# Optimization experiments

Hardware: AMD Instinct MI355X
Metric: run time of the kernel (lower is better)

The kernel has to match this reference:

```python
import jax, jax.numpy as jnp
import numpy as np

ALPHA = 1.702
LIMIT = 7.0


def setup_inputs() -> dict:
    key = jax.random.key(0)
    ks = jax.random.split(key, 6)
    A, B, E, M, H = 1, 1, 8, 1024, 2048
    I2 = 4096  # 2 * intermediate_size, interleaved gate/up
    inter = I2 // 2
    return {
        "dispatched": jax.random.normal(ks[0], (A, B, E, M, H), dtype=jnp.float32),
        "w1": jax.random.normal(ks[1], (E, H, I2), dtype=jnp.float32) * 0.02,
        "w1_bias": jax.random.normal(ks[2], (E, I2), dtype=jnp.float32) * 0.02,
        "w2": jax.random.normal(ks[3], (E, inter, H), dtype=jnp.float32) * 0.02,
        "w2_bias": jax.random.normal(ks[4], (E, H), dtype=jnp.float32) * 0.02,
        "sparsity_remap": jax.random.randint(ks[5], (E,), 0, E, dtype=jnp.int32),
        "BD": 1,
        "S": 1024,
    }


def reference(dispatched, w1, w1_bias, w2, w2_bias, sparsity_remap, BD, S):
    # dispatched: [A, B, E, M, H]; w1: [E, H, 2I]; w2: [E, I, H]
    # tt.sparse_matmul == grouped per-expert GEMM; dense math is identical.
    A, Bt, E, M, H = dispatched.shape
    # fused gate+up projection: [A, B, E, M, 2I]
    gu = jnp.einsum("abemh,ehn->abemn", dispatched, w1) + w1_bias[None, None, :, None, :]
    # interleaved gate/up split (gpt_oss activation path)
    gate = gu[..., 0::2]
    up = gu[..., 1::2]
    gate = jnp.minimum(gate, LIMIT)
    up = jnp.clip(up, -LIMIT, LIMIT)
    glu = gate * jax.nn.sigmoid(gate * ALPHA)
    activated = (up + 1.0) * glu  # [A, B, E, M, I]
    inter = activated.shape[-1]
    activated = activated.reshape(A * Bt, E, M, inter)
    # down projection: [A*B, E, M, H]
    down = jnp.einsum("bemi,eih->bemh", activated, w2) + w2_bias[None, :, None, :]
    # permute(1,0,2,3) then untile to [E, 1, BD*S, H]
    out = jnp.transpose(down, (1, 0, 2, 3)).reshape(E, 1, BD * S, H)
    return out
```

## Files before the change

### kernel.cpp

```cpp
#include <hip/hip_runtime.h>
#include <hip/hip_bf16.h>
#include <cstdint>
#include <cstddef>

#define E_ 8
#define M_ 1024
#define H_ 2048
#define I2_ 4096
#define INTER_ 2048

typedef __attribute__((ext_vector_type(8))) __bf16 bf16x8;
typedef __attribute__((ext_vector_type(4))) float f32x4;

__device__ __forceinline__ unsigned short f2bf(float x) {
  union { float f; unsigned u; } v; v.f = x;
  unsigned r = v.u + 0x7fffu + ((v.u >> 16) & 1u);
  return (unsigned short)(r >> 16);
}

__device__ __forceinline__ unsigned pk2(float lo, float hi) {
  __hip_bfloat162 h = __float22bfloat162_rn(make_float2(lo, hi));
  union { __hip_bfloat162 h2; unsigned u; } c; c.h2 = h; return c.u;
}

__device__ __forceinline__ int bofs(int kp, int r) {
  int f = (20 * ((kp >> 2) & 3)) ^ ((kp & 1) << 4);
  return kp * 128 + (r ^ f);
}

__global__ void k_cvt(const float* __restrict__ src, unsigned short* __restrict__ dst, int n4) {
  int i = blockIdx.x * blockDim.x + threadIdx.x;
  int stride = gridDim.x * blockDim.x;
  const float4* s4 = (const float4*)src;
  ushort4* d4 = (ushort4*)dst;
  for (; i < n4; i += stride) {
    float4 v = s4[i];
    ushort4 o;
    o.x = f2bf(v.x); o.y = f2bf(v.y); o.z = f2bf(v.z); o.w = f2bf(v.w);
    d4[i] = o;
  }
}

template<int PERM>
__global__ __launch_bounds__(256) void k_wt(
    const float* __restrict__ W, unsigned short* __restrict__ Wp, int Kd, int Nd) {
  __shared__ float tt[64][65];
  const int tid = threadIdx.x;
  const int e = blockIdx.z;
  const int nb0 = blockIdx.x * 64;
  const int k0 = blockIdx.y * 64;
  const float* We = W + (size_t)e * Kd * Nd;

  #pragma unroll
  for (int i = 0; i < 4; ++i) {
    int r = (tid >> 4) + 16 * i;
    int c4 = tid & 15;
    float4 v = *(const float4*)(We + (size_t)(k0 + r) * Nd + nb0 + 4 * c4);
    tt[r][4 * c4 + 0] = v.x;
    tt[r][4 * c4 + 1] = v.y;
    tt[r][4 * c4 + 2] = v.z;
    tt[r][4 * c4 + 3] = v.w;
  }
  __syncthreads();

  int n = tid >> 2;
  int kc = (tid & 3) * 16;
  int nglob = nb0 + n;
  int nrow;
  if (PERM) {
    int b = nglob >> 5, w = nglob & 31;
    nrow = 32 * b + ((w & 1) ? 16 + (w >> 1) : (w >> 1));
  } else {
    nrow = nglob;
  }
  unsigned o[8];
  #pragma unroll
  for (int j = 0; j < 8; ++j)
    o[j] = pk2(tt[kc + 2 * j][n], tt[kc + 2 * j + 1][n]);
  unsigned short* dst = Wp + (size_t)e * Nd * Kd + (size_t)nrow * Kd + k0 + kc;
  *(uint4*)(dst) = *(uint4*)&o[0];
  *(uint4*)(dst + 8) = *(uint4*)&o[4];
}

template<int ACT, int N, int K>
__global__ __launch_bounds__(256) void k_gemm_nt(
    const unsigned short* __restrict__ A,
    const unsigned short* __restrict__ B,
    const float* __restrict__ bias,
    unsigned short* __restrict__ ActOut,
    float* __restrict__ Out)
{
  __shared__ unsigned short la[128 * 64];
  __shared__ unsigned short lb[128 * 64];
  const int tid = threadIdx.x;
  const int lane = tid & 63;
  const int wv = tid >> 6;
  const int wm = wv & 1, wn = wv >> 1;
  const int e = blockIdx.z;
  const int n0 = blockIdx.x * 128;
  const int m0 = blockIdx.y * 128;
  const unsigned short* Ae = A + (size_t)e * M_ * K + (size_t)m0 * K;
  const unsigned short* Be = B + (size_t)e * N * K + (size_t)n0 * K;

  const unsigned short* ga[4];
  const unsigned short* gb[4];
  int seg[4];
  #pragma unroll
  for (int t = 0; t < 4; ++t) {
    int s = (wv * 4 + t) * 64 + lane;
    int m = s >> 3;
    int j = (s & 7) ^ (m & 7);
    ga[t] = Ae + (size_t)m * K + j * 8;
    gb[t] = Be + (size_t)m * K + j * 8;
    seg[t] = (wv * 4 + t) * 1024;
  }

  const int c = lane & 15;
  const int q = lane >> 4;

  f32x4 acc[4][4];
  const f32x4 zero = {0.f, 0.f, 0.f, 0.f};
  #pragma unroll
  for (int i = 0; i < 4; ++i)
    #pragma unroll
    for (int j = 0; j < 4; ++j) acc[i][j] = zero;

  const int KT = K / 64;
  for (int kt = 0; kt < KT; ++kt) {
    #pragma unroll
    for (int t = 0; t < 4; ++t) {
      __builtin_amdgcn_global_load_lds(
          (const __attribute__((address_space(1))) void*)(const void*)(ga[t] + kt * 64),
          (__attribute__((address_space(3))) void*)(void*)((char*)la + seg[t]), 16, 0, 0);
      __builtin_amdgcn_global_load_lds(
          (const __attribute__((address_space(1))) void*)(const void*)(gb[t] + kt * 64),
          (__attribute__((address_space(3))) void*)(void*)((char*)lb + seg[t]), 16, 0, 0);
    }
    __syncthreads();

    #pragma unroll
    for (int ks = 0; ks < 2; ++ks) {
      bf16x8 av[4], bv[4];
      #pragma unroll
      for (int mi = 0; mi < 4; ++mi) {
        int row = wm * 64 + mi * 16 + c;
        int slot = row * 8 + ((ks * 4 + q) ^ (c & 7));
        av[mi] = *(const bf16x8*)(la + slot * 8);
      }
      #pragma unroll
      for (int ni = 0; ni < 4; ++ni) {
        int row = wn * 64 + ni * 16 + c;
        int slot = row * 8 + ((ks * 4 + q) ^ (c & 7));
        bv[ni] = *(const bf16x8*)(lb + slot * 8);
      }
      #pragma unroll
      for (int mi = 0; mi < 4; ++mi)
        #pragma unroll
        for (int ni = 0; ni < 4; ++ni)
          acc[mi][ni] = __builtin_amdgcn_mfma_f32_16x16x32_bf16(av[mi], bv[ni], acc[mi][ni], 0, 0, 0);
    }
    __syncthreads();
  }

  if (ACT) {
    unsigned short* ActE = ActOut + (size_t)e * M_ * (N / 2);
    const float* be = bias + (size_t)e * N;
    int colbase = n0 + wn * 64;
    #pragma unroll
    for (int p = 0; p < 2; ++p) {
      int rgc = colbase + 32 * p + c;
      int norig = (rgc & ~31) | (c << 1);
      float bg_ = be[norig];
      float bu_ = be[norig + 1];
      int acol = ((rgc >> 5) << 4) + c;
      #pragma unroll
      for (int mi = 0; mi < 4; ++mi) {
        int rowb = m0 + wm * 64 + mi * 16 + q * 4;
        #pragma unroll
        for (int r = 0; r < 4; ++r) {
          float g = acc[mi][2 * p][r] + bg_;
          float u = acc[mi][2 * p + 1][r] + bu_;
          g = fminf(g, 7.0f);
          u = fminf(fmaxf(u, -7.0f), 7.0f);
          float glu = g / (1.0f + __expf(-1.702f * g));
          float a = (u + 1.0f) * glu;
          ActE[(size_t)(rowb + r) * (N / 2) + acol] = f2bf(a);
        }
      }
    }
  } else {
    float* OutE = Out + (size_t)e * M_ * N;
    const float* be = bias + (size_t)e * N;
    #pragma unroll
    for (int ni = 0; ni < 4; ++ni) {
      int col = n0 + wn * 64 + ni * 16 + c;
      float bb = be[col];
      #pragma unroll
      for (int mi = 0; mi < 4; ++mi) {
        int rowb = m0 + wm * 64 + mi * 16 + q * 4;
        #pragma unroll
        for (int r = 0; r < 4; ++r)
          OutE[(size_t)(rowb + r) * N + col] = acc[mi][ni][r] + bb;
      }
    }
  }
}

template<int ACT, int N, int K>
__global__ __launch_bounds__(256) void k_gemm(
    const unsigned short* __restrict__ A,
    const float* __restrict__ Bf,
    const float* __restrict__ bias,
    unsigned short* __restrict__ ActOut,
    float* __restrict__ Out)
{
  __shared__ unsigned short la[128 * 64];
  __shared__ unsigned lb32[32 * 128];
  const int tid = threadIdx.x;
  const int lane = tid & 63;
  const int wv = tid >> 6;
  const int wm = wv & 1, wn = wv >> 1;
  const int e = blockIdx.z;
  const int n0 = blockIdx.x * 128;
  const int m0 = blockIdx.y * 128;
  const unsigned short* Ae = A + (size_t)e * M_ * K + (size_t)m0 * K;
  const float* Be = Bf + (size_t)e * K * N + n0;

  const unsigned short* ga[4];
  int segb[4];
  #pragma unroll
  for (int t = 0; t < 4; ++t) {
    int s = (wv * 4 + t) * 64 + lane;
    int m = s >> 3;
    int j = (s & 7) ^ (m & 7);
    ga[t] = Ae + (size_t)m * K + j * 8;
    segb[t] = (wv * 4 + t) * 1024;
  }

  int kpb, colb, rg;
  if (ACT) {
    kpb = tid >> 4;
    int g = tid & 15;
    colb = 8 * g;
    rg = 32 * (g >> 2) + 4 * (g & 3);
  } else {
    kpb = tid >> 5;
    colb = 4 * (tid & 31);
    rg = colb;
  }
  const float* bg = Be + (size_t)(2 * kpb) * N + colb;

  const int c = lane & 15;
  const int q = lane >> 4;

  f32x4 acc[4][4];
  const f32x4 zero = {0.f, 0.f, 0.f, 0.f};
  #pragma unroll
  for (int i = 0; i < 4; ++i)
    #pragma unroll
    for (int j = 0; j < 4; ++j) acc[i][j] = zero;

  #define LD4(p, off) (*(const float4*)((p) + (off)))

  float4 pb[8];
  {
    const float* p = bg;
    if (ACT) {
      pb[0] = LD4(p, 0);                    pb[1] = LD4(p, 4);
      pb[2] = LD4(p, (size_t)N);            pb[3] = LD4(p, (size_t)N + 4);
      pb[4] = LD4(p, (size_t)32 * N);       pb[5] = LD4(p, (size_t)32 * N + 4);
      pb[6] = LD4(p, (size_t)33 * N);       pb[7] = LD4(p, (size_t)33 * N + 4);
    } else {
      #pragma unroll
      for (int uu = 0; uu < 4; ++uu) {
        pb[2 * uu]     = LD4(p, (size_t)(16 * uu) * N);
        pb[2 * uu + 1] = LD4(p, (size_t)(16 * uu + 1) * N);
      }
    }
  }

  const int KT = K / 64;
  for (int kt = 0; kt < KT; ++kt) {
    #pragma unroll
    for (int t = 0; t < 4; ++t) {
      __builtin_amdgcn_global_load_lds(
          (const __attribute__((address_space(1))) void*)(const void*)(ga[t] + kt * 64),
          (__attribute__((address_space(3))) void*)(void*)((char*)la + segb[t]), 16, 0, 0);
    }
    if (ACT) {
      #pragma unroll
      for (int uu = 0; uu < 2; ++uu) {
        int kp = kpb + 16 * uu;
        float4 a0 = pb[4 * uu], a1 = pb[4 * uu + 1], b0 = pb[4 * uu + 2], b1 = pb[4 * uu + 3];
        uint4 gv, uv;
        gv.x = pk2(a0.x, b0.x); gv.y = pk2(a0.z, b0.z); gv.z = pk2(a1.x, b1.x); gv.w = pk2(a1.z, b1.z);
        uv.x = pk2(a0.y, b0.y); uv.y = pk2(a0.w, b0.w); uv.z = pk2(a1.w, b1.w); uv.w = pk2(a1.w, b1.w);
        uv.z = pk2(a1.y, b1.y);
        *(uint4*)&lb32[bofs(kp, rg)] = gv;
        *(uint4*)&lb32[bofs(kp, rg + 16)] = uv;
      }
    } else {
      #pragma unroll
      for (int uu = 0; uu < 4; ++uu) {
        int kp = kpb + 8 * uu;
        float4 a = pb[2 * uu], b = pb[2 * uu + 1];
        uint4 v;
        v.x = pk2(a.x, b.x); v.y = pk2(a.y, b.y); v.z = pk2(a.z, b.z); v.w = pk2(a.w, b.w);
        *(uint4*)&lb32[bofs(kp, rg)] = v;
      }
    }
    __syncthreads();

    if (kt + 1 < KT) {
      const float* p = bg + (size_t)(kt + 1) * 64 * N;
      if (ACT) {
        pb[0] = LD4(p, 0);                    pb[1] = LD4(p, 4);
        pb[2] = LD4(p, (size_t)N);            pb[3] = LD4(p, (size_t)N + 4);
        pb[4] = LD4(p, (size_t)32 * N);       pb[5] = LD4(p, (size_t)32 * N + 4);
        pb[6] = LD4(p, (size_t)33 * N);       pb[7] = LD4(p, (size_t)33 * N + 4);
      } else {
        #pragma unroll
        for (int uu = 0; uu < 4; ++uu) {
          pb[2 * uu]     = LD4(p, (size_t)(16 * uu) * N);
          pb[2 * uu + 1] = LD4(p, (size_t)(16 * uu + 1) * N);
        }
      }
    }

    #pragma unroll
    for (int ks = 0; ks < 2; ++ks) {
      bf16x8 av[4], bv[4];
      #pragma unroll
      for (int mi = 0; mi < 4; ++mi) {
        int row = wm * 64 + mi * 16 + c;
        int slot = row * 8 + ((ks * 4 + q) ^ (c & 7));
        av[mi] = *(const bf16x8*)(la + slot * 8);
      }
      #pragma unroll
      for (int ni = 0; ni < 4; ++ni) {
        int r = wn * 64 + ni * 16 + c;
        union { unsigned u[4]; bf16x8 v; } t;
        #pragma unroll
        for (int jp = 0; jp < 4; ++jp)
          t.u[jp] = lb32[bofs(ks * 16 + q * 4 + jp, r)];
        bv[ni] = t.v;
      }
      #pragma unroll
      for (int mi = 0; mi < 4; ++mi)
        #pragma unroll
        for (int ni = 0; ni < 4; ++ni)
          acc[mi][ni] = __builtin_amdgcn_mfma_f32_16x16x32_bf16(av[mi], bv[ni], acc[mi][ni], 0, 0, 0);
    }
    __syncthreads();
  }
  #undef LD4

  if (ACT) {
    unsigned short* ActE = ActOut + (size_t)e * M_ * (N / 2);
    const float* be = bias + (size_t)e * N;
    int colbase = n0 + wn * 64;
    #pragma unroll
    for (int p = 0; p < 2; ++p) {
      int rgc = colbase + 32 * p + c;
      int norig = (rgc & ~31) | (c << 1);
      float bg_ = be[norig];
      float bu_ = be[norig + 1];
      int acol = ((rgc >> 5) << 4) + c;
      #pragma unroll
      for (int mi = 0; mi < 4; ++mi) {
        int rowb = m0 + wm * 64 + mi * 16 + q * 4;
        #pragma unroll
        for (int r = 0; r < 4; ++r) {
          float g = acc[mi][2 * p][r] + bg_;
          float u = acc[mi][2 * p + 1][r] + bu_;
          g = fminf(g, 7.0f);
          u = fminf(fmaxf(u, -7.0f), 7.0f);
          float glu = g / (1.0f + __expf(-1.702f * g));
          float a = (u + 1.0f) * glu;
          ActE[(size_t)(rowb + r) * (N / 2) + acol] = f2bf(a);
        }
      }
    }
  } else {
    float* OutE = Out + (size_t)e * M_ * N;
    const float* be = bias + (size_t)e * N;
    #pragma unroll
    for (int ni = 0; ni < 4; ++ni) {
      int col = n0 + wn * 64 + ni * 16 + c;
      float bb = be[col];
      #pragma unroll
      for (int mi = 0; mi < 4; ++mi) {
        int rowb = m0 + wm * 64 + mi * 16 + q * 4;
        #pragma unroll
        for (int r = 0; r < 4; ++r)
          OutE[(size_t)(rowb + r) * N + col] = acc[mi][ni][r] + bb;
      }
    }
  }
}

__global__ __launch_bounds__(256) void k_naive(const float* __restrict__ disp,
    const float* __restrict__ w1, const float* __restrict__ w1b,
    const float* __restrict__ w2, const float* __restrict__ w2b,
    float* __restrict__ out) {
  __shared__ float xrow[H_];
  __shared__ float act[INTER_];
  int b = blockIdx.x;
  int e = b / M_;
  int m = b % M_;
  const float* x = disp + (size_t)(e * M_ + m) * H_;
  int tid = threadIdx.x;
  for (int k = tid; k < H_; k += 256) xrow[k] = x[k];
  __syncthreads();
  const float* w1e = w1 + (size_t)e * H_ * I2_;
  const float* b1e = w1b + (size_t)e * I2_;
  for (int jj = 0; jj < INTER_ / 256; ++jj) {
    int i = tid + jj * 256;
    float g = b1e[2 * i], u = b1e[2 * i + 1];
    for (int k = 0; k < H_; ++k) {
      float xv = xrow[k];
      g += xv * w1e[(size_t)k * I2_ + 2 * i];
      u += xv * w1e[(size_t)k * I2_ + 2 * i + 1];
    }
    g = fminf(g, 7.0f);
    u = fminf(fmaxf(u, -7.0f), 7.0f);
    float glu = g / (1.0f + __expf(-1.702f * g));
    act[i] = (u + 1.0f) * glu;
  }
  __syncthreads();
  const float* w2e = w2 + (size_t)e * INTER_ * H_;
  const float* b2e = w2b + (size_t)e * H_;
  float* oute = out + (size_t)(e * M_ + m) * H_;
  for (int jj = 0; jj < H_ / 256; ++jj) {
    int h = tid + jj * 256;
    float o = b2e[h];
    for (int i = 0; i < INTER_; ++i) o += act[i] * w2e[(size_t)i * H_ + h];
    oute[h] = o;
  }
}

extern "C" void kernel_launch(void* const* d_in, const int* in_sizes, int n_in,
                              void* d_out, int out_size, void* d_ws, size_t ws_size,
                              hipStream_t stream) {
  const float* disp = (const float*)d_in[0];
  const float* w1   = (const float*)d_in[1];
  const float* w1b  = (const float*)d_in[2];
  const float* w2   = (const float*)d_in[3];
  const float* w2b  = (const float*)d_in[4];
  float* out = (float*)d_out;

  const size_t nA   = (size_t)E_ * M_ * H_;
  const size_t nAct = (size_t)E_ * M_ * INTER_;
  const size_t nW1  = (size_t)E_ * I2_ * H_;
  const size_t nW2  = (size_t)E_ * H_ * INTER_;
  const size_t need_full = (nA + nAct + nW1 + nW2) * 2;
  const size_t need_old  = (nA + nAct) * 2;

  if (ws_size >= need_full) {
    unsigned short* actb = (unsigned short*)d_ws;
    unsigned short* ab   = actb + nAct;
    unsigned short* w1p  = ab + nA;
    unsigned short* w2p  = w1p + nW1;

    k_cvt<<<4096, 256, 0, stream>>>(disp, ab, (int)(nA / 4));
    k_wt<1><<<dim3(I2_ / 64, H_ / 64, E_), 256, 0, stream>>>(w1, w1p, H_, I2_);
    k_wt<0><<<dim3(H_ / 64, INTER_ / 64, E_), 256, 0, stream>>>(w2, w2p, INTER_, H_);
    k_gemm_nt<1, I2_, H_><<<dim3(I2_ / 128, M_ / 128, E_), 256, 0, stream>>>(ab, w1p, w1b, actb, nullptr);
    k_gemm_nt<0, H_, INTER_><<<dim3(H_ / 128, M_ / 128, E_), 256, 0, stream>>>(actb, w2p, w2b, nullptr, out);
  } else if (ws_size >= need_old) {
    unsigned short* actb = (unsigned short*)d_ws;
    unsigned short* ab   = actb + nAct;

    k_cvt<<<4096, 256, 0, stream>>>(disp, ab, (int)(nA / 4));
    k_gemm<1, I2_, H_><<<dim3(I2_ / 128, M_ / 128, E_), 256, 0, stream>>>(ab, w1, w1b, actb, nullptr);
    k_gemm<0, H_, INTER_><<<dim3(H_ / 128, M_ / 128, E_), 256, 0, stream>>>(actb, w2, w2b, nullptr, out);
  } else {
    k_naive<<<E_ * M_, 256, 0, stream>>>(disp, w1, w1b, w2, w2b, out);
  }
}
```

Measured before the change: 831.3 us.

## Double-buffer LDS tiles in bf16 NT GEMM to overlap global loads with MFMA

Doubles the LDS buffers in k_gemm_nt and restructures the K loop as a ping-pong pipeline. The next tile's global_load_lds is issued before computing on the current tile, so load latency overlaps with MFMA work. LDS read offsets are precomputed, and s_setprio raises wave priority during compute. This doubles LDS use to 64KB per block, which may lower occupancy. The loop assumes KT is even, and it also cleans up a redundant pk2 assignment.

New measurement: 820.8 us. Within noise of the previous version (-1.3%).

```diff
diff --git a/kernel.cpp b/kernel.cpp
--- a/kernel.cpp
+++ b/kernel.cpp
@@ -82,6 +82,38 @@
   *(uint4*)(dst + 8) = *(uint4*)&o[4];
 }
 
+__device__ __forceinline__ void stage_tile(
+    const unsigned short* const (&ga)[4], const unsigned short* const (&gb)[4],
+    const int (&seg)[4], char* laB, char* lbB, int kt) {
+  #pragma unroll
+  for (int t = 0; t < 4; ++t) {
+    __builtin_amdgcn_global_load_lds(
+        (const __attribute__((address_space(1))) void*)(const void*)(ga[t] + kt * 64),
+        (__attribute__((address_space(3))) void*)(void*)(laB + seg[t]), 16, 0, 0);
+    __builtin_amdgcn_global_load_lds(
+        (const __attribute__((address_space(1))) void*)(const void*)(gb[t] + kt * 64),
+        (__attribute__((address_space(3))) void*)(void*)(lbB + seg[t]), 16, 0, 0);
+  }
+}
+
+__device__ __forceinline__ void compute_tile(
+    const unsigned short* laB, const unsigned short* lbB,
+    const int (&slA)[2][4], const int (&slB)[2][4], f32x4 (&acc)[4][4]) {
+  #pragma unroll
+  for (int ks = 0; ks < 2; ++ks) {
+    bf16x8 av[4], bv[4];
+    #pragma unroll
+    for (int mi = 0; mi < 4; ++mi) av[mi] = *(const bf16x8*)(laB + slA[ks][mi]);
+    #pragma unroll
+    for (int ni = 0; ni < 4; ++ni) bv[ni] = *(const bf16x8*)(lbB + slB[ks][ni]);
+    #pragma unroll
+    for (int mi = 0; mi < 4; ++mi)
+      #pragma unroll
+      for (int ni = 0; ni < 4; ++ni)
+        acc[mi][ni] = __builtin_amdgcn_mfma_f32_16x16x32_bf16(av[mi], bv[ni], acc[mi][ni], 0, 0, 0);
+  }
+}
+
 template<int ACT, int N, int K>
 __global__ __launch_bounds__(256) void k_gemm_nt(
     const unsigned short* __restrict__ A,
@@ -90,8 +122,8 @@
     unsigned short* __restrict__ ActOut,
     float* __restrict__ Out)
 {
-  __shared__ unsigned short la[128 * 64];
-  __shared__ unsigned short lb[128 * 64];
+  __shared__ unsigned short la[2][128 * 64];
+  __shared__ unsigned short lb[2][128 * 64];
   const int tid = threadIdx.x;
   const int lane = tid & 63;
   const int wv = tid >> 6;
@@ -118,6 +150,17 @@
   const int c = lane & 15;
   const int q = lane >> 4;
 
+  int slA[2][4], slB[2][4];
+  #pragma unroll
+  for (int ks = 0; ks < 2; ++ks) {
+    #pragma unroll
+    for (int i = 0; i < 4; ++i) {
+      int xorj = (ks * 4 + q) ^ (c & 7);
+      slA[ks][i] = ((wm * 64 + i * 16 + c) * 8 + xorj) * 8;
+      slB[ks][i] = ((wn * 64 + i * 16 + c) * 8 + xorj) * 8;
+    }
+  }
+
   f32x4 acc[4][4];
   const f32x4 zero = {0.f, 0.f, 0.f, 0.f};
   #pragma unroll
@@ -126,40 +169,23 @@
     for (int j = 0; j < 4; ++j) acc[i][j] = zero;
 
   const int KT = K / 64;
-  for (int kt = 0; kt < KT; ++kt) {
-    #pragma unroll
-    for (int t = 0; t < 4; ++t) {
-      __builtin_amdgcn_global_load_lds(
-          (const __attribute__((address_space(1))) void*)(const void*)(ga[t] + kt * 64),
-          (__attribute__((address_space(3))) void*)(void*)((char*)la + seg[t]), 16, 0, 0);
-      __builtin_amdgcn_global_load_lds(
-          (const __attribute__((address_space(1))) void*)(const void*)(gb[t] + kt * 64),
-          (__attribute__((address_space(3))) void*)(void*)((char*)lb + seg[t]), 16, 0, 0);
-    }
-    __syncthreads();
-
-    #pragma unroll
-    for (int ks = 0; ks < 2; ++ks) {
-      bf16x8 av[4], bv[4];
-      #pragma unroll
-      for (int mi = 0; mi < 4; ++mi) {
-        int row = wm * 64 + mi * 16 + c;
-        int slot = row * 8 + ((ks * 4 + q) ^ (c & 7));
-        av[mi] = *(const bf16x8*)(la + slot * 8);
-      }
-      #pragma unroll
-      for (int ni = 0; ni < 4; ++ni) {
-        int row = wn * 64 + ni * 16 + c;
-        int slot = row * 8 + ((ks * 4 + q) ^ (c & 7));
-        bv[ni] = *(const bf16x8*)(lb + slot * 8);
-      }
-      #pragma unroll
-      for (int mi = 0; mi < 4; ++mi)
-        #pragma unroll
-        for (int ni = 0; ni < 4; ++ni)
-          acc[mi][ni] = __builtin_amdgcn_mfma_f32_16x16x32_bf16(av[mi], bv[ni], acc[mi][ni], 0, 0, 0);
-    }
-    __syncthreads();
+  stage_tile(ga, gb, seg, (char*)&la[0][0], (char*)&lb[0][0], 0);
+  asm volatile("s_waitcnt vmcnt(0)\n\ts_barrier" ::: "memory");
+
+  for (int kt = 0; kt < KT; kt += 2) {
+    if (kt + 1 < KT)
+      stage_tile(ga, gb, seg, (char*)&la[1][0], (char*)&lb[1][0], kt + 1);
+    __builtin_amdgcn_s_setprio(1);
+    compute_tile(&la[0][0], &lb[0][0], slA, slB, acc);
+    __builtin_amdgcn_s_setprio(0);
+    asm volatile("s_waitcnt vmcnt(0)\n\ts_barrier" ::: "memory");
+
+    if (kt + 2 < KT)
+      stage_tile(ga, gb, seg, (char*)&la[0][0], (char*)&lb[0][0], kt + 2);
+    __builtin_amdgcn_s_setprio(1);
+    compute_tile(&la[1][0], &lb[1][0], slA, slB, acc);
+    __builtin_amdgcn_s_setprio(0);
+    asm volatile("s_waitcnt vmcnt(0)\n\ts_barrier" ::: "memory");
   }
 
   if (ACT) {
@@ -294,8 +320,7 @@
         float4 a0 = pb[4 * uu], a1 = pb[4 * uu + 1], b0 = pb[4 * uu + 2], b1 = pb[4 * uu + 3];
         uint4 gv, uv;
         gv.x = pk2(a0.x, b0.x); gv.y = pk2(a0.z, b0.z); gv.z = pk2(a1.x, b1.x); gv.w = pk2(a1.z, b1.z);
-        uv.x = pk2(a0.y, b0.y); uv.y = pk2(a0.w, b0.w); uv.z = pk2(a1.w, b1.w); uv.w = pk2(a1.w, b1.w);
-        uv.z = pk2(a1.y, b1.y);
+        uv.x = pk2(a0.y, b0.y); uv.y = pk2(a0.w, b0.w); uv.z = pk2(a1.y, b1.y); uv.w = pk2(a1.w, b1.w);
         *(uint4*)&lb32[bofs(kp, rg)] = gv;
         *(uint4*)&lb32[bofs(kp, rg + 16)] = uv;
       }
```
